# Kernel tuning notes

Hardware: AMD Instinct MI355X
Metric: run time of the kernel (lower is better)

## Reference

```python
import jax, jax.numpy as jnp
import numpy as np

N_NODES = 50000
N_EDGES = 400000
IN_C, HID, EDGE_D = 128, 256, 32
NUM_LAYERS = 3

def _gnblock(x, src, dst, edge_attr, ew, eb, nw, nb):
    # edge message MLP: relu(W [x_src, x_dst, e] + b)  -> [E, HID]
    m = jax.nn.relu(jnp.concatenate([x[src], x[dst], edge_attr], axis=-1) @ ew + eb)
    # mean aggregation by destination node
    agg = jax.ops.segment_sum(m, dst, num_segments=N_NODES)
    deg = jax.ops.segment_sum(jnp.ones((m.shape[0],), m.dtype), dst, num_segments=N_NODES)
    agg = agg / jnp.maximum(deg, 1.0)[:, None]
    # node update MLP: relu(W [x, agg] + b) -> [N, HID]
    return jax.nn.relu(jnp.concatenate([x, agg], axis=-1) @ nw + nb)

def setup_inputs() -> dict:
    key = jax.random.key(0)
    ks = jax.random.split(key, 12)
    s = 0.05  # keep activations sane
    return {
        'x': jax.random.normal(ks[0], (N_NODES, IN_C), jnp.float32),
        'edge_index': jax.random.randint(ks[1], (2, N_EDGES), 0, N_NODES, jnp.int32),
        'edge_attr': jax.random.normal(ks[2], (N_EDGES, EDGE_D), jnp.float32),
        'e0_w': jax.random.normal(ks[3], (2 * IN_C + EDGE_D, HID), jnp.float32) * s,
        'e0_b': jnp.zeros((HID,), jnp.float32),
        'n0_w': jax.random.normal(ks[4], (IN_C + HID, HID), jnp.float32) * s,
        'n0_b': jnp.zeros((HID,), jnp.float32),
        'e_w': jax.random.normal(ks[5], (NUM_LAYERS - 1, 2 * HID + EDGE_D, HID), jnp.float32) * s,
        'e_b': jnp.zeros((NUM_LAYERS - 1, HID), jnp.float32),
        'n_w': jax.random.normal(ks[6], (NUM_LAYERS - 1, 2 * HID, HID), jnp.float32) * s,
        'n_b': jnp.zeros((NUM_LAYERS - 1, HID), jnp.float32),
        'h1_w': jax.random.normal(ks[7], (HID, HID), jnp.float32) * s,
        'h1_b': jnp.zeros((HID,), jnp.float32),
        'h2_w': jax.random.normal(ks[8], (HID, 1), jnp.float32) * s,
        'h2_b': jnp.zeros((1,), jnp.float32),
    }

def reference(x, edge_index, edge_attr, e0_w, e0_b, n0_w, n0_b,
              e_w, e_b, n_w, n_b, h1_w, h1_b, h2_w, h2_b):
    src, dst = edge_index[0], edge_index[1]
    h = _gnblock(x, src, dst, edge_attr, e0_w, e0_b, n0_w, n0_b)
    for i in range(NUM_LAYERS - 1):
        h = _gnblock(h, src, dst, edge_attr, e_w[i], e_b[i], n_w[i], n_b[i])
    # MLP head -> per-node logit [N, 1]
    h = jax.nn.relu(h @ h1_w + h1_b)
    return h @ h2_w + h2_b
```

## Files before the change

kernel.cpp:

```cpp
#include <hip/hip_runtime.h>
#include <hip/hip_bf16.h>
#include <hip/hip_fp16.h>

#define NN 50000
#define NE 400000
#define NBLK 196

typedef unsigned short u16;
typedef unsigned int u32;
typedef __attribute__((ext_vector_type(8))) short short8;
typedef __attribute__((ext_vector_type(4))) float f32x4;
typedef __attribute__((ext_vector_type(4))) unsigned short u16x4;
typedef __attribute__((ext_vector_type(2))) _Float16 h2;

typedef __attribute__((address_space(1))) const void as1_void;
typedef __attribute__((address_space(3))) void as3_void;

static __device__ __forceinline__ float bf2f(u16 u) {
    return __uint_as_float(((u32)u) << 16);
}
static __device__ __forceinline__ u16 f2bf(float f) {
    u32 x = __float_as_uint(f);
    x += 0x7fffu + ((x >> 16) & 1u);
    return (u16)(x >> 16);
}
static __device__ __forceinline__ u32 packh2(float a, float b) {
    return ((u32)__half_as_ushort(__float2half(b)) << 16) |
           (u32)__half_as_ushort(__float2half(a));
}
static __device__ __forceinline__ float fdot2u(u32 a, u32 b, float c) {
    return __builtin_amdgcn_fdot2(__builtin_bit_cast(h2, a),
                                  __builtin_bit_cast(h2, b), c, false);
}

static __device__ __forceinline__ void gload_lds16(const u16* g, u16* l) {
    __builtin_amdgcn_global_load_lds((as1_void*)g, (as3_void*)l, 16, 0, 0);
}

__global__ __launch_bounds__(256) void gemm_bt(
    const u16* __restrict__ A, int lda,
    const u16* __restrict__ Bt,
    u16* __restrict__ C, int ldc,
    int M, int K,
    const float* __restrict__ bias,
    const u16* __restrict__ aux, int ld_aux,
    int relu)
{
    __shared__ u16 As[128 * 32];
    __shared__ u16 Bs[128 * 32];

    const int t = threadIdx.x;
    const int w = t >> 6;
    const int lane = t & 63;
    const int quad = lane >> 4;
    const int l15 = lane & 15;
    const int tile_m = blockIdx.x * 128;
    const int tile_n = blockIdx.y * 128;
    const int wm = (w >> 1) * 64;
    const int wn = (w & 1) * 64;

    f32x4 acc[4][4];
#pragma unroll
    for (int r = 0; r < 4; ++r)
#pragma unroll
        for (int c = 0; c < 4; ++c)
            acc[r][c] = (f32x4){0.f, 0.f, 0.f, 0.f};

    int ar0 = tile_m + (t >> 2);      if (ar0 > M - 1) ar0 = M - 1;
    int ar1 = tile_m + 64 + (t >> 2); if (ar1 > M - 1) ar1 = M - 1;
    const int br0 = tile_n + (t >> 2);
    const int br1 = tile_n + 64 + (t >> 2);
    const int koff = (t & 3) * 8;

    u16* lAs0 = As + w * 512;
    u16* lAs1 = As + 2048 + w * 512;
    u16* lBs0 = Bs + w * 512;
    u16* lBs1 = Bs + 2048 + w * 512;

    const u16* Arow0 = A + (size_t)ar0 * lda + koff;
    const u16* Arow1 = A + (size_t)ar1 * lda + koff;
    const u16* Brow0 = Bt + (size_t)br0 * K + koff;
    const u16* Brow1 = Bt + (size_t)br1 * K + koff;

    for (int k0 = 0; k0 < K; k0 += 32) {
        gload_lds16(Arow0 + k0, lAs0);
        gload_lds16(Arow1 + k0, lAs1);
        gload_lds16(Brow0 + k0, lBs0);
        gload_lds16(Brow1 + k0, lBs1);
        __syncthreads();

        short8 af[4], bfr[4];
#pragma unroll
        for (int r = 0; r < 4; ++r)
            af[r] = *(const short8*)&As[(wm + r * 16 + l15) * 32 + quad * 8];
#pragma unroll
        for (int c = 0; c < 4; ++c)
            bfr[c] = *(const short8*)&Bs[(wn + c * 16 + l15) * 32 + quad * 8];
#pragma unroll
        for (int r = 0; r < 4; ++r)
#pragma unroll
            for (int c = 0; c < 4; ++c)
                acc[r][c] = __builtin_amdgcn_mfma_f32_16x16x32_bf16(af[r], bfr[c], acc[r][c], 0, 0, 0);
        __syncthreads();
    }

#pragma unroll
    for (int r = 0; r < 4; ++r) {
#pragma unroll
        for (int c = 0; c < 4; ++c) {
            const int coln = tile_n + wn + c * 16 + l15;
            const float bv = bias ? bias[coln] : 0.0f;
#pragma unroll
            for (int i = 0; i < 4; ++i) {
                const int row = tile_m + wm + r * 16 + quad * 4 + i;
                if (row < M) {
                    float v = acc[r][c][i] + bv;
                    if (aux) v += bf2f(aux[(size_t)row * ld_aux + coln]);
                    if (relu) v = fmaxf(v, 0.f);
                    C[(size_t)row * ldc + coln] = f2bf(v);
                }
            }
        }
    }
}

__global__ __launch_bounds__(256) void edge_agg_fused(
    const u16* __restrict__ P,
    const u32* __restrict__ eattr_p32,
    const u32* __restrict__ WePk,
    const int* __restrict__ row_start,
    const int* __restrict__ src_perm,
    const float* __restrict__ inv_deg,
    const float* __restrict__ eb,
    u16* __restrict__ agg)
{
    const int node = (int)((blockIdx.x * 256 + threadIdx.x) >> 6);
    const int lane = threadIdx.x & 63;
    const int l15 = lane & 15;
    const int col = lane * 4;

    uint4 wpk[16];
#pragma unroll
    for (int kp = 0; kp < 16; ++kp)
        wpk[kp] = *(const uint4*)(WePk + kp * 256 + col);

    u16x4 pdv = *(const u16x4*)(P + (size_t)node * 768 + 256 + col);
    f32x4 pb;
    pb[0] = bf2f(pdv[0]) + eb[col];
    pb[1] = bf2f(pdv[1]) + eb[col + 1];
    pb[2] = bf2f(pdv[2]) + eb[col + 2];
    pb[3] = bf2f(pdv[3]) + eb[col + 3];

    f32x4 accv = (f32x4){0.f, 0.f, 0.f, 0.f};
    const int s0r = row_start[node], s1r = row_start[node + 1];

    if (s1r > s0r) {
        const int jlast = s1r - 1;
        int j1 = (s0r + 1 < jlast) ? s0r + 1 : jlast;
        int sa = src_perm[s0r];
        int sb = src_perm[j1];
        u16x4 psa = *(const u16x4*)(P + (size_t)sa * 768 + col);
        u16x4 psb = *(const u16x4*)(P + (size_t)sb * 768 + col);
        u32 eva = eattr_p32[(size_t)s0r * 16 + l15];
        u32 evb = eattr_p32[(size_t)j1 * 16 + l15];

        for (int j = s0r; j < s1r; ++j) {
            int jc = (j + 2 < jlast) ? j + 2 : jlast;
            int sn = src_perm[jc];
            u16x4 psn = *(const u16x4*)(P + (size_t)sn * 768 + col);
            u32 evn = eattr_p32[(size_t)jc * 16 + l15];

            f32x4 q = pb;
#pragma unroll
            for (int kp = 0; kp < 16; ++kp) {
                u32 evk = (u32)__builtin_amdgcn_readlane((int)eva, kp);
                q[0] = fdot2u(evk, wpk[kp].x, q[0]);
                q[1] = fdot2u(evk, wpk[kp].y, q[1]);
                q[2] = fdot2u(evk, wpk[kp].z, q[2]);
                q[3] = fdot2u(evk, wpk[kp].w, q[3]);
            }
            q[0] += bf2f(psa[0]);
            q[1] += bf2f(psa[1]);
            q[2] += bf2f(psa[2]);
            q[3] += bf2f(psa[3]);
            accv[0] += fmaxf(q[0], 0.f);
            accv[1] += fmaxf(q[1], 0.f);
            accv[2] += fmaxf(q[2], 0.f);
            accv[3] += fmaxf(q[3], 0.f);

            psa = psb; eva = evb;
            psb = psn; evb = evn;
        }
    }

    const float idg = inv_deg[node];
    u16x4 o;
    o[0] = f2bf(accv[0] * idg);
    o[1] = f2bf(accv[1] * idg);
    o[2] = f2bf(accv[2] * idg);
    o[3] = f2bf(accv[3] * idg);
    *(u16x4*)(agg + (size_t)node * 256 + col) = o;
}

__global__ __launch_bounds__(256) void head_out(
    const u16* __restrict__ h3,
    const float* __restrict__ h2w,
    const float* __restrict__ h2b,
    float* __restrict__ out)
{
    const int node = (int)((blockIdx.x * 256 + threadIdx.x) >> 6);
    const int lane = threadIdx.x & 63;
    if (node >= NN) return;
    const int col = lane * 4;
    u16x4 hv = *(const u16x4*)(h3 + (size_t)node * 256 + col);
    float4 wv = *(const float4*)(h2w + col);
    float s = bf2f(hv[0]) * wv.x + bf2f(hv[1]) * wv.y +
              bf2f(hv[2]) * wv.z + bf2f(hv[3]) * wv.w;
    for (int off = 32; off > 0; off >>= 1)
        s += __shfl_down(s, off, 64);
    if (lane == 0) out[node] = s + h2b[0];
}

__global__ void zero_int(int* p, int n) {
    int i = blockIdx.x * 256 + threadIdx.x;
    if (i < n) p[i] = 0;
}

__global__ void hist_k(const int* __restrict__ ei, int* __restrict__ deg) {
    int e = blockIdx.x * 256 + threadIdx.x;
    if (e < NE) atomicAdd(&deg[ei[NE + e]], 1);
}

__global__ __launch_bounds__(256) void block_sum_k(const int* __restrict__ deg,
                                                   int* __restrict__ bsum) {
    __shared__ int sm[4];
    const int i = blockIdx.x * 256 + threadIdx.x;
    int v = (i < NN) ? deg[i] : 0;
    for (int off = 32; off > 0; off >>= 1)
        v += __shfl_down(v, off, 64);
    const int lane = threadIdx.x & 63;
    const int w = threadIdx.x >> 6;
    if (lane == 0) sm[w] = v;
    __syncthreads();
    if (threadIdx.x == 0)
        bsum[blockIdx.x] = sm[0] + sm[1] + sm[2] + sm[3];
}

__global__ __launch_bounds__(256) void scan_block_k(const int* __restrict__ bsum,
                                                    int* __restrict__ boff,
                                                    int* __restrict__ row_start) {
    __shared__ int sm[256];
    const int tid = threadIdx.x;
    int v = (tid < NBLK) ? bsum[tid] : 0;
    sm[tid] = v;
    __syncthreads();
    for (int o = 1; o < 256; o <<= 1) {
        int tv = (tid >= o) ? sm[tid - o] : 0;
        __syncthreads();
        sm[tid] += tv;
        __syncthreads();
    }
    if (tid < NBLK) boff[tid] = sm[tid] - v;
    if (tid == NBLK - 1) row_start[NN] = sm[tid];
}

__global__ __launch_bounds__(256) void writeback_k(const int* __restrict__ deg,
                                                   const int* __restrict__ boff,
                                                   int* __restrict__ row_start,
                                                   int* __restrict__ cursor,
                                                   float* __restrict__ inv_deg) {
    __shared__ int sm[256];
    const int tid = threadIdx.x;
    const int i = blockIdx.x * 256 + tid;
    int v = (i < NN) ? deg[i] : 0;
    sm[tid] = v;
    __syncthreads();
    for (int o = 1; o < 256; o <<= 1) {
        int tv = (tid >= o) ? sm[tid - o] : 0;
        __syncthreads();
        sm[tid] += tv;
        __syncthreads();
    }
    if (i < NN) {
        const int rs = boff[blockIdx.x] + sm[tid] - v;
        row_start[i] = rs;
        cursor[i]    = rs;
        inv_deg[i]   = 1.0f / fmaxf((float)v, 1.0f);
    }
}

__global__ void scatter_k(const int* __restrict__ ei, const float* __restrict__ eattr,
                          int* __restrict__ cursor, int* __restrict__ src_perm,
                          u32* __restrict__ eattr_p32) {
    int e = blockIdx.x * 256 + threadIdx.x;
    if (e >= NE) return;
    int s = ei[e], d = ei[NE + e];
    int pos = atomicAdd(&cursor[d], 1);
    src_perm[pos] = s;
    const float* sr = eattr + (size_t)e * 32;
    u32* dr = eattr_p32 + (size_t)pos * 16;
#pragma unroll
    for (int j = 0; j < 16; ++j)
        dr[j] = packh2(sr[2 * j], sr[2 * j + 1]);
}

struct TJob { const float* src; u16* dst; int K; int ksh; int tr; };
struct TJobs { TJob j[16]; };

__global__ void transpose_k(TJobs jobs) {
    TJob jb = jobs.j[blockIdx.y];
    int idx = blockIdx.x * 256 + threadIdx.x;
    if (idx >= (jb.K << 8)) return;
    if (jb.tr == 1) {
        int n = idx >> jb.ksh;
        int k = idx & (jb.K - 1);
        jb.dst[idx] = f2bf(jb.src[k * 256 + n]);
    } else {
        int kp = idx >> 8;
        int c = idx & 255;
        ((u32*)jb.dst)[idx] = packh2(jb.src[(2 * kp) * 256 + c],
                                     jb.src[(2 * kp + 1) * 256 + c]);
    }
}

__global__ void cvt_f32_bf16(const float* __restrict__ src, u16* __restrict__ dst, int n) {
    int i = blockIdx.x * 256 + threadIdx.x;
    if (i < n) dst[i] = f2bf(src[i]);
}

extern "C" void kernel_launch(void* const* d_in, const int* in_sizes, int n_in,
                              void* d_out, int out_size, void* d_ws, size_t ws_size,
                              hipStream_t stream) {
    const float* x     = (const float*)d_in[0];
    const int*   ei    = (const int*)d_in[1];
    const float* eattr = (const float*)d_in[2];
    const float* e0_w  = (const float*)d_in[3];
    const float* e0_b  = (const float*)d_in[4];
    const float* n0_w  = (const float*)d_in[5];
    const float* n0_b  = (const float*)d_in[6];
    const float* e_w   = (const float*)d_in[7];
    const float* e_b   = (const float*)d_in[8];
    const float* n_w   = (const float*)d_in[9];
    const float* n_b   = (const float*)d_in[10];
    const float* h1_w  = (const float*)d_in[11];
    const float* h1_b  = (const float*)d_in[12];
    const float* h2_w  = (const float*)d_in[13];
    const float* h2_b  = (const float*)d_in[14];
    float* out = (float*)d_out;
    (void)in_sizes; (void)n_in; (void)out_size; (void)ws_size;

    char* base = (char*)d_ws;
    size_t off = 0;
    auto alloc = [&](size_t nbytes) -> void* {
        void* p = base + off;
        off += (nbytes + 255) & ~(size_t)255;
        return p;
    };

    int*   deg       = (int*)alloc(NN * 4);
    int*   row_start = (int*)alloc((NN + 1) * 4);
    int*   cursor    = (int*)alloc(NN * 4);
    float* invdeg    = (float*)alloc(NN * 4);
    int*   bsum      = (int*)alloc(NBLK * 4);
    int*   boff      = (int*)alloc(NBLK * 4);
    int*   src_perm  = (int*)alloc(NE * 4);
    u32*   eattr_p32 = (u32*)alloc((size_t)NE * 16 * 4);
    u16*   WcatT0    = (u16*)alloc(768 * 128 * 2);
    u16*   WcatT1    = (u16*)alloc(768 * 256 * 2);
    u16*   WcatT2    = (u16*)alloc(768 * 256 * 2);
    u32*   WePk0     = (u32*)alloc(16 * 256 * 4);
    u32*   WePk1     = (u32*)alloc(16 * 256 * 4);
    u32*   WePk2     = (u32*)alloc(16 * 256 * 4);
    u16*   NbT0      = (u16*)alloc(256 * 256 * 2);
    u16*   NbT1      = (u16*)alloc(256 * 256 * 2);
    u16*   NbT2      = (u16*)alloc(256 * 256 * 2);
    u16*   H1T       = (u16*)alloc(256 * 256 * 2);
    u16*   P         = (u16*)alloc((size_t)NN * 768 * 2);
    u16*   aggb      = (u16*)alloc((size_t)NN * 256 * 2);
    u16*   hb        = (u16*)alloc((size_t)NN * 256 * 2);
    u16*   xb        = aggb;

    zero_int<<<(NN + 255) / 256, 256, 0, stream>>>(deg, NN);
    hist_k<<<(NE + 255) / 256, 256, 0, stream>>>(ei, deg);
    block_sum_k<<<NBLK, 256, 0, stream>>>(deg, bsum);
    scan_block_k<<<1, 256, 0, stream>>>(bsum, boff, row_start);
    writeback_k<<<NBLK, 256, 0, stream>>>(deg, boff, row_start, cursor, invdeg);
    scatter_k<<<(NE + 255) / 256, 256, 0, stream>>>(ei, eattr, cursor, src_perm, eattr_p32);

    const float* ew2 = e_w + 544 * 256;
    const float* nw2 = n_w + 512 * 256;

    TJobs tj;
    auto setj = [&](int i, const float* s, void* d, int K, int tr) {
        tj.j[i].src = s; tj.j[i].dst = (u16*)d; tj.j[i].K = K; tj.j[i].tr = tr;
        tj.j[i].ksh = (K == 256) ? 8 : (K == 128 ? 7 : 5);
    };
    setj(0,  e0_w,             WcatT0,             128, 1);
    setj(1,  e0_w + 128 * 256, WcatT0 + 256 * 128, 128, 1);
    setj(2,  n0_w,             WcatT0 + 512 * 128, 128, 1);
    setj(3,  n0_w + 128 * 256, NbT0,               256, 1);
    setj(4,  e_w,              WcatT1,             256, 1);
    setj(5,  e_w + 256 * 256,  WcatT1 + 256 * 256, 256, 1);
    setj(6,  n_w,              WcatT1 + 512 * 256, 256, 1);
    setj(7,  n_w + 256 * 256,  NbT1,               256, 1);
    setj(8,  ew2,              WcatT2,             256, 1);
    setj(9,  ew2 + 256 * 256,  WcatT2 + 256 * 256, 256, 1);
    setj(10, nw2,              WcatT2 + 512 * 256, 256, 1);
    setj(11, nw2 + 256 * 256,  NbT2,               256, 1);
    setj(12, h1_w,             H1T,                256, 1);
    setj(13, e0_w + 256 * 256, WePk0,              16,  2);
    setj(14, e_w + 512 * 256,  WePk1,              16,  2);
    setj(15, ew2 + 512 * 256,  WePk2,              16,  2);
    transpose_k<<<dim3(256, 16), 256, 0, stream>>>(tj);

    cvt_f32_bf16<<<(NN * 128 + 255) / 256, 256, 0, stream>>>(x, xb, NN * 128);

    const int MT = (NN + 127) / 128;
    u16* WcatT[3] = {WcatT0, WcatT1, WcatT2};
    u32* WePk[3]  = {WePk0, WePk1, WePk2};
    u16* NbT[3]   = {NbT0, NbT1, NbT2};
    const float* ebs[3] = {e0_b, e_b, e_b + 256};
    const float* nbs[3] = {n0_b, n_b, n_b + 256};

    for (int l = 0; l < 3; ++l) {
        const u16* hin = (l == 0) ? xb : hb;
        const int kin = (l == 0) ? 128 : 256;
        gemm_bt<<<dim3(MT, 6), 256, 0, stream>>>(hin, kin, WcatT[l], P, 768, NN, kin,
                                                 nullptr, nullptr, 0, 0);
        edge_agg_fused<<<NN / 4, 256, 0, stream>>>(P, eattr_p32, WePk[l], row_start,
                                                   src_perm, invdeg, ebs[l], aggb);
        gemm_bt<<<dim3(MT, 2), 256, 0, stream>>>(aggb, 256, NbT[l], hb, 256, NN, 256,
                                                 nbs[l], P + 512, 768, 1);
    }
    gemm_bt<<<dim3(MT, 2), 256, 0, stream>>>(hb, 256, H1T, aggb, 256, NN, 256,
                                             h1_b, nullptr, 0, 1);
    head_out<<<NN / 4, 256, 0, stream>>>(aggb, h2_w, h2_b, out);
}
```

Before: 938.9 us.

## Concatenate agg and h in a Z buffer to fuse node-update GEMM

```diff
diff --git a/kernel.cpp b/kernel.cpp
--- a/kernel.cpp
+++ b/kernel.cpp
@@ -43,7 +43,6 @@
     u16* __restrict__ C, int ldc,
     int M, int K,
     const float* __restrict__ bias,
-    const u16* __restrict__ aux, int ld_aux,
     int relu)
 {
     __shared__ u16 As[128 * 32];
@@ -115,7 +114,6 @@
                 const int row = tile_m + wm + r * 16 + quad * 4 + i;
                 if (row < M) {
                     float v = acc[r][c][i] + bv;
-                    if (aux) v += bf2f(aux[(size_t)row * ld_aux + coln]);
                     if (relu) v = fmaxf(v, 0.f);
                     C[(size_t)row * ldc + coln] = f2bf(v);
                 }
@@ -131,25 +129,25 @@
     const int* __restrict__ row_start,
     const int* __restrict__ src_perm,
     const float* __restrict__ inv_deg,
-    const float* __restrict__ eb,
-    u16* __restrict__ agg)
+    u16* __restrict__ aggZ)
 {
     const int node = (int)((blockIdx.x * 256 + threadIdx.x) >> 6);
     const int lane = threadIdx.x & 63;
     const int l15 = lane & 15;
     const int col = lane * 4;
+    if (node >= NN) return;
 
     uint4 wpk[16];
 #pragma unroll
     for (int kp = 0; kp < 16; ++kp)
         wpk[kp] = *(const uint4*)(WePk + kp * 256 + col);
 
-    u16x4 pdv = *(const u16x4*)(P + (size_t)node * 768 + 256 + col);
+    u16x4 pdv = *(const u16x4*)(P + (size_t)node * 512 + 256 + col);
     f32x4 pb;
-    pb[0] = bf2f(pdv[0]) + eb[col];
-    pb[1] = bf2f(pdv[1]) + eb[col + 1];
-    pb[2] = bf2f(pdv[2]) + eb[col + 2];
-    pb[3] = bf2f(pdv[3]) + eb[col + 3];
+    pb[0] = bf2f(pdv[0]);
+    pb[1] = bf2f(pdv[1]);
+    pb[2] = bf2f(pdv[2]);
+    pb[3] = bf2f(pdv[3]);
 
     f32x4 accv = (f32x4){0.f, 0.f, 0.f, 0.f};
     const int s0r = row_start[node], s1r = row_start[node + 1];
@@ -159,15 +157,15 @@
         int j1 = (s0r + 1 < jlast) ? s0r + 1 : jlast;
         int sa = src_perm[s0r];
         int sb = src_perm[j1];
-        u16x4 psa = *(const u16x4*)(P + (size_t)sa * 768 + col);
-        u16x4 psb = *(const u16x4*)(P + (size_t)sb * 768 + col);
+        u16x4 psa = *(const u16x4*)(P + (size_t)sa * 512 + col);
+        u16x4 psb = *(const u16x4*)(P + (size_t)sb * 512 + col);
         u32 eva = eattr_p32[(size_t)s0r * 16 + l15];
         u32 evb = eattr_p32[(size_t)j1 * 16 + l15];
 
         for (int j = s0r; j < s1r; ++j) {
             int jc = (j + 2 < jlast) ? j + 2 : jlast;
             int sn = src_perm[jc];
-            u16x4 psn = *(const u16x4*)(P + (size_t)sn * 768 + col);
+            u16x4 psn = *(const u16x4*)(P + (size_t)sn * 512 + col);
             u32 evn = eattr_p32[(size_t)jc * 16 + l15];
 
             f32x4 q = pb;
@@ -199,11 +197,11 @@
     o[1] = f2bf(accv[1] * idg);
     o[2] = f2bf(accv[2] * idg);
     o[3] = f2bf(accv[3] * idg);
-    *(u16x4*)(agg + (size_t)node * 256 + col) = o;
+    *(u16x4*)(aggZ + (size_t)node * 512 + col) = o;
 }
 
 __global__ __launch_bounds__(256) void head_out(
-    const u16* __restrict__ h3,
+    const u16* __restrict__ h4Z,
     const float* __restrict__ h2w,
     const float* __restrict__ h2b,
     float* __restrict__ out)
@@ -212,7 +210,7 @@
     const int lane = threadIdx.x & 63;
     if (node >= NN) return;
     const int col = lane * 4;
-    u16x4 hv = *(const u16x4*)(h3 + (size_t)node * 256 + col);
+    u16x4 hv = *(const u16x4*)(h4Z + (size_t)node * 512 + col);
     float4 wv = *(const float4*)(h2w + col);
     float s = bf2f(hv[0]) * wv.x + bf2f(hv[1]) * wv.y +
               bf2f(hv[2]) * wv.z + bf2f(hv[3]) * wv.w;
@@ -304,7 +302,18 @@
         dr[j] = packh2(sr[2 * j], sr[2 * j + 1]);
 }
 
-struct TJob { const float* src; u16* dst; int K; int ksh; int tr; };
+__global__ void bias_build(const float* __restrict__ e0b,
+                           const float* __restrict__ eb1,
+                           const float* __restrict__ eb2,
+                           float* __restrict__ dst) {
+    int i = blockIdx.x * 256 + threadIdx.x;
+    if (i >= 1536) return;
+    int l = i >> 9, c = i & 511;
+    const float* s = (l == 0) ? e0b : (l == 1) ? eb1 : eb2;
+    dst[i] = (c < 256) ? 0.f : s[c - 256];
+}
+
+struct TJob { const float* src; u16* dst; int K; int ksh; int tr; int dstride; };
 struct TJobs { TJob j[16]; };
 
 __global__ void transpose_k(TJobs jobs) {
@@ -314,7 +323,7 @@
     if (jb.tr == 1) {
         int n = idx >> jb.ksh;
         int k = idx & (jb.K - 1);
-        jb.dst[idx] = f2bf(jb.src[k * 256 + n]);
+        jb.dst[n * jb.dstride + k] = f2bf(jb.src[k * 256 + n]);
     } else {
         int kp = idx >> 8;
         int c = idx & 255;
@@ -323,9 +332,11 @@
     }
 }
 
-__global__ void cvt_f32_bf16(const float* __restrict__ src, u16* __restrict__ dst, int n) {
+__global__ void cvt_x(const float* __restrict__ src, u16* __restrict__ Z) {
     int i = blockIdx.x * 256 + threadIdx.x;
-    if (i < n) dst[i] = f2bf(src[i]);
+    if (i >= NN * 128) return;
+    int n = i >> 7, c = i & 127;
+    Z[(size_t)n * 512 + 256 + c] = f2bf(src[i]);
 }
 
 extern "C" void kernel_launch(void* const* d_in, const int* in_sizes, int n_in,
@@ -365,20 +376,20 @@
     int*   boff      = (int*)alloc(NBLK * 4);
     int*   src_perm  = (int*)alloc(NE * 4);
     u32*   eattr_p32 = (u32*)alloc((size_t)NE * 16 * 4);
-    u16*   WcatT0    = (u16*)alloc(768 * 128 * 2);
-    u16*   WcatT1    = (u16*)alloc(768 * 256 * 2);
-    u16*   WcatT2    = (u16*)alloc(768 * 256 * 2);
+    u16*   WcatT0    = (u16*)alloc(512 * 128 * 2);
+    u16*   WcatT1    = (u16*)alloc(512 * 256 * 2);
+    u16*   WcatT2    = (u16*)alloc(512 * 256 * 2);
     u32*   WePk0     = (u32*)alloc(16 * 256 * 4);
     u32*   WePk1     = (u32*)alloc(16 * 256 * 4);
     u32*   WePk2     = (u32*)alloc(16 * 256 * 4);
-    u16*   NbT0      = (u16*)alloc(256 * 256 * 2);
-    u16*   NbT1      = (u16*)alloc(256 * 256 * 2);
-    u16*   NbT2      = (u16*)alloc(256 * 256 * 2);
+    u16*   BcatT0    = (u16*)alloc(256 * 384 * 2);
+    u16*   BcatT1    = (u16*)alloc(256 * 512 * 2);
+    u16*   BcatT2    = (u16*)alloc(256 * 512 * 2);
     u16*   H1T       = (u16*)alloc(256 * 256 * 2);
-    u16*   P         = (u16*)alloc((size_t)NN * 768 * 2);
-    u16*   aggb      = (u16*)alloc((size_t)NN * 256 * 2);
-    u16*   hb        = (u16*)alloc((size_t)NN * 256 * 2);
-    u16*   xb        = aggb;
+    float* bias512   = (float*)alloc(3 * 512 * 4);
+    u16*   P         = (u16*)alloc((size_t)NN * 512 * 2);
+    u16*   Z0        = (u16*)alloc((size_t)NN * 512 * 2);
+    u16*   Z1        = (u16*)alloc((size_t)NN * 512 * 2);
 
     zero_int<<<(NN + 255) / 256, 256, 0, stream>>>(deg, NN);
     hist_k<<<(NE + 255) / 256, 256, 0, stream>>>(ei, deg);
@@ -386,53 +397,56 @@
     scan_block_k<<<1, 256, 0, stream>>>(bsum, boff, row_start);
     writeback_k<<<NBLK, 256, 0, stream>>>(deg, boff, row_start, cursor, invdeg);
     scatter_k<<<(NE + 255) / 256, 256, 0, stream>>>(ei, eattr, cursor, src_perm, eattr_p32);
+    bias_build<<<6, 256, 0, stream>>>(e0_b, e_b, e_b + 256, bias512);
 
     const float* ew2 = e_w + 544 * 256;
     const float* nw2 = n_w + 512 * 256;
 
     TJobs tj;
-    auto setj = [&](int i, const float* s, void* d, int K, int tr) {
+    auto setj = [&](int i, const float* s, void* d, int K, int tr, int dstride) {
         tj.j[i].src = s; tj.j[i].dst = (u16*)d; tj.j[i].K = K; tj.j[i].tr = tr;
+        tj.j[i].dstride = dstride;
         tj.j[i].ksh = (K == 256) ? 8 : (K == 128 ? 7 : 5);
     };
-    setj(0,  e0_w,             WcatT0,             128, 1);
-    setj(1,  e0_w + 128 * 256, WcatT0 + 256 * 128, 128, 1);
-    setj(2,  n0_w,             WcatT0 + 512 * 128, 128, 1);
-    setj(3,  n0_w + 128 * 256, NbT0,               256, 1);
-    setj(4,  e_w,              WcatT1,             256, 1);
-    setj(5,  e_w + 256 * 256,  WcatT1 + 256 * 256, 256, 1);
-    setj(6,  n_w,              WcatT1 + 512 * 256, 256, 1);
-    setj(7,  n_w + 256 * 256,  NbT1,               256, 1);
-    setj(8,  ew2,              WcatT2,             256, 1);
-    setj(9,  ew2 + 256 * 256,  WcatT2 + 256 * 256, 256, 1);
-    setj(10, nw2,              WcatT2 + 512 * 256, 256, 1);
-    setj(11, nw2 + 256 * 256,  NbT2,               256, 1);
-    setj(12, h1_w,             H1T,                256, 1);
-    setj(13, e0_w + 256 * 256, WePk0,              16,  2);
-    setj(14, e_w + 512 * 256,  WePk1,              16,  2);
-    setj(15, ew2 + 512 * 256,  WePk2,              16,  2);
+    setj(0,  e0_w,             WcatT0,             128, 1, 128);
+    setj(1,  e0_w + 128 * 256, WcatT0 + 256 * 128, 128, 1, 128);
+    setj(2,  e_w,              WcatT1,             256, 1, 256);
+    setj(3,  e_w + 256 * 256,  WcatT1 + 256 * 256, 256, 1, 256);
+    setj(4,  ew2,              WcatT2,             256, 1, 256);
+    setj(5,  ew2 + 256 * 256,  WcatT2 + 256 * 256, 256, 1, 256);
+    setj(6,  n0_w + 128 * 256, BcatT0,             256, 1, 384);
+    setj(7,  n0_w,             BcatT0 + 256,       128, 1, 384);
+    setj(8,  n_w + 256 * 256,  BcatT1,             256, 1, 512);
+    setj(9,  n_w,              BcatT1 + 256,       256, 1, 512);
+    setj(10, nw2 + 256 * 256,  BcatT2,             256, 1, 512);
+    setj(11, nw2,              BcatT2 + 256,       256, 1, 512);
+    setj(12, h1_w,             H1T,                256, 1, 256);
+    setj(13, e0_w + 256 * 256, WePk0,              16,  2, 0);
+    setj(14, e_w + 512 * 256,  WePk1,              16,  2, 0);
+    setj(15, ew2 + 512 * 256,  WePk2,              16,  2, 0);
     transpose_k<<<dim3(256, 16), 256, 0, stream>>>(tj);
 
-    cvt_f32_bf16<<<(NN * 128 + 255) / 256, 256, 0, stream>>>(x, xb, NN * 128);
+    cvt_x<<<(NN * 128 + 255) / 256, 256, 0, stream>>>(x, Z0);
 
     const int MT = (NN + 127) / 128;
     u16* WcatT[3] = {WcatT0, WcatT1, WcatT2};
     u32* WePk[3]  = {WePk0, WePk1, WePk2};
-    u16* NbT[3]   = {NbT0, NbT1, NbT2};
-    const float* ebs[3] = {e0_b, e_b, e_b + 256};
+    u16* BcatT[3] = {BcatT0, BcatT1, BcatT2};
     const float* nbs[3] = {n0_b, n_b, n_b + 256};
+    u16* Zin[3]  = {Z0, Z1, Z0};
+    u16* Zout[3] = {Z1, Z0, Z1};
+    const int kin[3]  = {128, 256, 256};
+    const int knode[3] = {384, 512, 512};
 
     for (int l = 0; l < 3; ++l) {
-        const u16* hin = (l == 0) ? xb : hb;
-        const int kin = (l == 0) ? 128 : 256;
-        gemm_bt<<<dim3(MT, 6), 256, 0, stream>>>(hin, kin, WcatT[l], P, 768, NN, kin,
-                                                 nullptr, nullptr, 0, 0);
+        gemm_bt<<<dim3(MT, 4), 256, 0, stream>>>(Zin[l] + 256, 512, WcatT[l], P, 512,
+                                                 NN, kin[l], bias512 + l * 512, 0);
         edge_agg_fused<<<NN / 4, 256, 0, stream>>>(P, eattr_p32, WePk[l], row_start,
-                                                   src_perm, invdeg, ebs[l], aggb);
-        gemm_bt<<<dim3(MT, 2), 256, 0, stream>>>(aggb, 256, NbT[l], hb, 256, NN, 256,
-                                                 nbs[l], P + 512, 768, 1);
-    }
-    gemm_bt<<<dim3(MT, 2), 256, 0, stream>>>(hb, 256, H1T, aggb, 256, NN, 256,
-                                             h1_b, nullptr, 0, 1);
-    head_out<<<NN / 4, 256, 0, stream>>>(aggb, h2_w, h2_b, out);
-}
+                                                   src_perm, invdeg, Zin[l]);
+        gemm_bt<<<dim3(MT, 2), 256, 0, stream>>>(Zin[l], 512, BcatT[l], Zout[l] + 256, 512,
+                                                 NN, knode[l], nbs[l], 1);
+    }
+    gemm_bt<<<dim3(MT, 2), 256, 0, stream>>>(Z1 + 256, 512, H1T, Z1, 512,
+                                             NN, 256, h1_b, 1);
+    head_out<<<NN / 4, 256, 0, stream>>>(Z1, h2_w, h2_b, out);
+}
```

Result: faster. 870.3 us (-7.3%).
